# Kernel tuning notes

Hardware: AMD Instinct MI355X
Metric: run time of the kernel (lower is better)

## Reference

```python
import jax, jax.numpy as jnp
import numpy as np

# dims: num_time T, batch B, nodes N, feature F(=hidden_dim), heads H(must be 1, see notes)
T, B, N, F, H = 16, 32, 512, 128, 1
E = F * T          # embed_size = hidden_dim * num_time = 2048
D = E // H         # head_dim = 2048


def setup_inputs() -> dict:
    key = jax.random.key(0)
    ks = jax.random.split(key, 9)
    s = 0.02
    return {
        "x":   jax.random.normal(ks[0], (T, B, N, F), dtype=jnp.float32),
        # torch nn.Linear convention: W is [out_features, in_features], y = x @ W.T + b
        "Wq":  jax.random.normal(ks[1], (D, D), dtype=jnp.float32) * s,
        "bq":  jnp.zeros((D,), dtype=jnp.float32),
        "Wk":  jax.random.normal(ks[2], (D, D), dtype=jnp.float32) * s,
        "bk":  jnp.zeros((D,), dtype=jnp.float32),
        "Wv":  jax.random.normal(ks[3], (E, D), dtype=jnp.float32) * s,
        "bv":  jnp.zeros((E,), dtype=jnp.float32),
        "Wfc": jax.random.normal(ks[4], (E, E), dtype=jnp.float32) * s,
        "bfc": jnp.zeros((E,), dtype=jnp.float32),
    }


def reference(x, Wq, bq, Wk, bk, Wv, bv, Wfc, bfc):
    Tt, Bb, Nn, Ff = x.shape
    Ee = Ff * Tt
    # mean over axis 1 of the ORIGINAL [T,B,N,F] tensor (this is the batch axis;
    # the original code calls it node_axis but operates on the un-permuted x)
    x_mean = x.mean(axis=1)                                   # [T, N, F]
    # permute(1,2,3,0).reshape -> [B, N, F*T], then split heads (H=1)
    xr = jnp.transpose(x, (1, 2, 3, 0)).reshape(Bb, Nn, H, Ee // H)
    q = xr @ Wq.T + bq                                        # [B, N, H, D]
    k = xr @ Wk.T + bk                                        # [B, N, H, D]
    v = xr @ Wv.T + bv                                        # [B, N, H, E]
    energy = jnp.einsum('nqhd,nkhd->nhqk', q, k)              # [B, H, N, N]
    attention = jax.nn.softmax(energy / jnp.sqrt(jnp.float32(Ee)), axis=3)
    out = jnp.einsum('nhql,nlhd->nqhd', attention, v).reshape(Bb, Nn, Ee)
    out = out @ Wfc.T + bfc                                   # [B, N, E]
    # faithful to the original's (buggy) view: (nodes, batch, T, F) then permute
    out = jnp.transpose(out.reshape(Nn, Bb, Tt, Ff), (2, 1, 0, 3)).mean(axis=1)  # [T, N, F]
    return x_mean + out, attention
```

## Files before the change

### kernel.cpp

```cpp
#include <hip/hip_runtime.h>

typedef __attribute__((ext_vector_type(8))) __bf16 bf16x8;
typedef __attribute__((ext_vector_type(4))) float floatx4;

__device__ __forceinline__ float bf2f(unsigned short u) {
    union { unsigned int i; float f; } v; v.i = ((unsigned int)u) << 16; return v.f;
}
__device__ __forceinline__ unsigned short f2bf(float f) {
    union { float f; unsigned int i; } v; v.f = f;
    unsigned int u = v.i;
    return (unsigned short)((u + 0x7fffu + ((u >> 16) & 1u)) >> 16);
}

__device__ __forceinline__ void async16(const void* g, void* l) {
    __builtin_amdgcn_global_load_lds(
        (__attribute__((address_space(1))) void*)(g),
        (__attribute__((address_space(3))) void*)(l), 16, 0, 0);
}

__global__ void detect_dtype(const unsigned short* __restrict__ w, int* __restrict__ flag)
{
    int tid = threadIdx.x;
    int cnt = 0;
    for (int i = tid; i < 256; i += 64) {
        unsigned short s = w[2 * i];
        int e = (s >> 7) & 0xFF;
        if (e >= 100 && e <= 126) cnt++;
    }
#pragma unroll
    for (int off = 32; off > 0; off >>= 1) cnt += __shfl_xor(cnt, off);
    if (tid == 0) *flag = (cnt >= 128) ? 1 : 0;
}

__global__ __launch_bounds__(256)
void convert_bf16(const void* __restrict__ in, unsigned short* __restrict__ out,
                  int n, float scale, const int* __restrict__ flag)
{
    int i = (blockIdx.x * 256 + threadIdx.x) * 4;
    if (i >= n) return;
    float f[4];
    if (*flag) {
        const unsigned short* p = (const unsigned short*)in + i;
#pragma unroll
        for (int j = 0; j < 4; j++) f[j] = bf2f(p[j]);
    } else {
        float4 v = *(const float4*)((const float*)in + i);
        f[0] = v.x; f[1] = v.y; f[2] = v.z; f[3] = v.w;
    }
    union { uint2 u; unsigned short s[4]; } W;
#pragma unroll
    for (int j = 0; j < 4; j++) W.s[j] = f2bf(f[j] * scale);
    *(uint2*)(out + i) = W.u;
}

__global__ __launch_bounds__(256)
void transpose_conv(const void* __restrict__ in, unsigned short* __restrict__ out,
                    const int* __restrict__ flag)
{
    __shared__ unsigned short tile[64 * 65];
    const int d0 = blockIdx.x * 64, i0 = blockIdx.y * 64;
    const int tid = threadIdx.x;
    const int r = tid >> 2, seg = tid & 3;

    const long base = (long)(d0 + r) * 2048 + i0 + seg * 16;
    unsigned short vals[16];
    if (*flag) {
        const unsigned short* p = (const unsigned short*)in + base;
        union { uint4 u; unsigned short s[8]; } a, b;
        a.u = *(const uint4*)p; b.u = *(const uint4*)(p + 8);
#pragma unroll
        for (int j = 0; j < 8; j++) { vals[j] = a.s[j]; vals[8 + j] = b.s[j]; }
    } else {
        const float* p = (const float*)in + base;
#pragma unroll
        for (int q = 0; q < 4; q++) {
            float4 v = *(const float4*)(p + q * 4);
            vals[q * 4 + 0] = f2bf(v.x); vals[q * 4 + 1] = f2bf(v.y);
            vals[q * 4 + 2] = f2bf(v.z); vals[q * 4 + 3] = f2bf(v.w);
        }
    }
#pragma unroll
    for (int j = 0; j < 16; j++) tile[r * 65 + seg * 16 + j] = vals[j];
    __syncthreads();

    union { uint4 u[2]; unsigned short s[16]; } W;
#pragma unroll
    for (int j = 0; j < 16; j++) W.s[j] = tile[(seg * 16 + j) * 65 + r];
    unsigned short* o = out + (long)(i0 + r) * 2048 + d0 + seg * 16;
    *(uint4*)o = W.u[0];
    *(uint4*)(o + 8) = W.u[1];
}

__global__ __launch_bounds__(256)
void build_xr(const void* __restrict__ xv, unsigned short* __restrict__ xr,
              const int* __restrict__ flag)
{
    __shared__ __align__(16) unsigned short tile[128 * 24];
    const int bn = blockIdx.x;
    const int b = bn >> 9, n = bn & 511;
    const int tid = threadIdx.x;
    const int t = tid >> 4, l16 = tid & 15;

    const long off = (long)(t * 32 + b) * 65536 + n * 128 + l16 * 8;
    union { uint4 u; unsigned short s[8]; } U;
    if (*flag) {
        U.u = *(const uint4*)((const unsigned short*)xv + off);
    } else {
        const float* xf = (const float*)xv + off;
        float4 f0 = *(const float4*)xf;
        float4 f1 = *(const float4*)(xf + 4);
        U.s[0] = f2bf(f0.x); U.s[1] = f2bf(f0.y); U.s[2] = f2bf(f0.z); U.s[3] = f2bf(f0.w);
        U.s[4] = f2bf(f1.x); U.s[5] = f2bf(f1.y); U.s[6] = f2bf(f1.z); U.s[7] = f2bf(f1.w);
    }
#pragma unroll
    for (int j = 0; j < 8; j++) tile[(l16 * 8 + j) * 24 + t] = U.s[j];
    __syncthreads();

    const int f = tid >> 1, t0 = (tid & 1) * 8;
    uint4 o = *(const uint4*)&tile[f * 24 + t0];
    *(uint4*)(xr + (long)bn * 2048 + tid * 8) = o;
}

template <int MODE, bool BIAS>
__global__ __launch_bounds__(256)
void gemm_nt(const unsigned short* __restrict__ Ag,
             const unsigned short* __restrict__ Bg,
             void* __restrict__ Cg,
             const unsigned short* __restrict__ bias,
             int K, long sA, long sB, long sC, int lda, int ldb, int ldc)
{
    __shared__ __align__(16) unsigned short lsA[128 * 32];
    __shared__ __align__(16) unsigned short lsB[128 * 32];

    const int tid = threadIdx.x;
    const int z = blockIdx.z;
    const unsigned short* A = Ag + (long)z * sA + (long)blockIdx.y * 128 * lda;
    const unsigned short* B = Bg + (long)z * sB + (long)blockIdx.x * 128 * ldb;

    const int wave = tid >> 6, lane = tid & 63;
    const int wm = (wave >> 1) * 64, wn = (wave & 1) * 64;
    const int r = lane & 15, quad = lane >> 4;

    floatx4 acc[4][4];
#pragma unroll
    for (int i = 0; i < 4; i++)
#pragma unroll
        for (int j = 0; j < 4; j++) acc[i][j] = floatx4{0.f, 0.f, 0.f, 0.f};

    const int srow = tid >> 2;
    const int scol = (tid & 3) * 8;
    const long a0 = (long)srow * lda + scol;
    const long a1 = (long)(srow + 64) * lda + scol;
    const long b0 = (long)srow * ldb + scol;
    const long b1 = (long)(srow + 64) * ldb + scol;

    for (int k0 = 0; k0 < K; k0 += 32) {
        async16(A + k0 + a0, (char*)lsA + tid * 16);
        async16(A + k0 + a1, (char*)lsA + 4096 + tid * 16);
        async16(B + k0 + b0, (char*)lsB + tid * 16);
        async16(B + k0 + b1, (char*)lsB + 4096 + tid * 16);
        __syncthreads();

        const bf16x8* pA = (const bf16x8*)lsA;
        const bf16x8* pB = (const bf16x8*)lsB;
        bf16x8 af[4], bb[4];
#pragma unroll
        for (int i = 0; i < 4; i++) af[i] = pA[(wm + i * 16 + r) * 4 + quad];
#pragma unroll
        for (int j = 0; j < 4; j++) bb[j] = pB[(wn + j * 16 + r) * 4 + quad];
#pragma unroll
        for (int i = 0; i < 4; i++)
#pragma unroll
            for (int j = 0; j < 4; j++)
                acc[i][j] = __builtin_amdgcn_mfma_f32_16x16x32_bf16(af[i], bb[j], acc[i][j], 0, 0, 0);
        __syncthreads();
    }

    const int mb = blockIdx.y * 128 + wm + quad * 4;
    const int nb = blockIdx.x * 128 + wn + r;

    if (MODE == 1) {
        float* C = (float*)Cg + (long)z * sC;
#pragma unroll
        for (int i = 0; i < 4; i++)
#pragma unroll
            for (int j = 0; j < 4; j++)
#pragma unroll
                for (int g = 0; g < 4; g++)
                    C[(long)(mb + i * 16 + g) * ldc + (nb + j * 16)] = acc[i][j][g];
    } else {
        unsigned short* C = (unsigned short*)Cg + (long)z * sC;
#pragma unroll
        for (int j = 0; j < 4; j++) {
            const int n = nb + j * 16;
            const float bj = BIAS ? bf2f(bias[n]) : 0.0f;
#pragma unroll
            for (int i = 0; i < 4; i++)
#pragma unroll
                for (int g = 0; g < 4; g++)
                    C[(long)(mb + i * 16 + g) * ldc + n] = f2bf(acc[i][j][g] + bj);
        }
    }
}

__global__ __launch_bounds__(256)
void w2_kernel(const unsigned short* __restrict__ WkT,
               const unsigned short* __restrict__ bqb, float* __restrict__ w2)
{
    const int i = blockIdx.x, tid = threadIdx.x;
    const unsigned short* row = WkT + (long)i * 2048 + tid * 8;
    const unsigned short* bv = bqb + tid * 8;
    union { uint4 u; unsigned short s[8]; } A, B;
    A.u = *(const uint4*)row; B.u = *(const uint4*)bv;
    float s = 0.f;
#pragma unroll
    for (int j = 0; j < 8; j++) s += bf2f(A.s[j]) * bf2f(B.s[j]);
#pragma unroll
    for (int off = 32; off > 0; off >>= 1) s += __shfl_xor(s, off);
    __shared__ float red[4];
    if ((tid & 63) == 0) red[tid >> 6] = s;
    __syncthreads();
    if (tid == 0) w2[i] = red[0] + red[1] + red[2] + red[3];
}

__global__ __launch_bounds__(256)
void c_kernel(const unsigned short* __restrict__ xr, const float* __restrict__ w2,
              float* __restrict__ c)
{
    const int row = blockIdx.x * 4 + (threadIdx.x >> 6);
    const int lane = threadIdx.x & 63;
    float s = 0.f;
#pragma unroll
    for (int ch = 0; ch < 4; ch++) {
        const int i0 = ch * 512 + lane * 8;
        union { uint4 u; unsigned short s[8]; } X;
        X.u = *(const uint4*)(xr + (long)row * 2048 + i0);
        float4 w0 = *(const float4*)(w2 + i0);
        float4 w1 = *(const float4*)(w2 + i0 + 4);
        s += bf2f(X.s[0]) * w0.x + bf2f(X.s[1]) * w0.y + bf2f(X.s[2]) * w0.z + bf2f(X.s[3]) * w0.w;
        s += bf2f(X.s[4]) * w1.x + bf2f(X.s[5]) * w1.y + bf2f(X.s[6]) * w1.z + bf2f(X.s[7]) * w1.w;
    }
#pragma unroll
    for (int off = 32; off > 0; off >>= 1) s += __shfl_xor(s, off);
    if (lane == 0) c[row] = s;
}

__global__ __launch_bounds__(256)
void softmax_rows(const float* __restrict__ S, const float* __restrict__ c,
                  void* __restrict__ dout, const int* __restrict__ flag)
{
    const long row = blockIdx.x;
    const int tid = threadIdx.x;
    const float scale = 0.02209708691207961f;
    float2 v = ((const float2*)(S + row * 512))[tid];
    float2 cv = ((const float2*)(c + (row >> 9) * 512))[tid];
    float a = (v.x + cv.x) * scale, b = (v.y + cv.y) * scale;

    __shared__ float redm[4], reds[4];
    float m = fmaxf(a, b);
#pragma unroll
    for (int off = 32; off > 0; off >>= 1) m = fmaxf(m, __shfl_xor(m, off));
    if ((tid & 63) == 0) redm[tid >> 6] = m;
    __syncthreads();
    m = fmaxf(fmaxf(redm[0], redm[1]), fmaxf(redm[2], redm[3]));

    float ea = __expf(a - m), eb = __expf(b - m);
    float s = ea + eb;
#pragma unroll
    for (int off = 32; off > 0; off >>= 1) s += __shfl_xor(s, off);
    if ((tid & 63) == 0) reds[tid >> 6] = s;
    __syncthreads();
    s = reds[0] + reds[1] + reds[2] + reds[3];
    const float inv = 1.0f / s;
    const float fa = ea * inv, fb = eb * inv;

    if (*flag) {
        unsigned short* P = (unsigned short*)dout + 1048576;
        const unsigned int packed = (unsigned int)f2bf(fa) | ((unsigned int)f2bf(fb) << 16);
        ((unsigned int*)(P + row * 512))[tid] = packed;
    } else {
        float* P = (float*)dout + 1048576;
        ((float2*)(P + row * 512))[tid] = make_float2(fa, fb);
    }
}

__global__ __launch_bounds__(256)
void pbar_reduce(const void* __restrict__ dout, unsigned short* __restrict__ Pbar,
                 const int* __restrict__ flag)
{
    const int g = blockIdx.x, tid = threadIdx.x;
    float s0 = 0.f, s1 = 0.f;
    if (*flag) {
        const unsigned short* P = (const unsigned short*)dout + 1048576;
        const unsigned short* p = P + (long)g * 32 * 512 + tid * 2;
        for (int r = 0; r < 32; r++) {
            unsigned int u = *(const unsigned int*)(p + (long)r * 512);
            s0 += bf2f((unsigned short)(u & 0xffff));
            s1 += bf2f((unsigned short)(u >> 16));
        }
    } else {
        const float* P = (const float*)dout + 1048576;
        const float* p = P + (long)g * 32 * 512 + tid * 2;
        for (int r = 0; r < 32; r++) {
            float2 v = *(const float2*)(p + (long)r * 512);
            s0 += v.x; s1 += v.y;
        }
    }
    const unsigned int packed = (unsigned int)f2bf(s0) | ((unsigned int)f2bf(s1) << 16);
    ((unsigned int*)(Pbar + (long)g * 512))[tid] = packed;
}

__global__ __launch_bounds__(256)
void z_kernel(const unsigned short* __restrict__ Pbar,
              const unsigned short* __restrict__ xr,
              unsigned short* __restrict__ Z)
{
    __shared__ __align__(16) unsigned short tile[32 * 64];
    const int b = blockIdx.y, d0 = blockIdx.x * 64;
    const int tid = threadIdx.x;
    const int wave = tid >> 6, lane = tid & 63;
    const int r = lane & 15, quad = lane >> 4;
    const unsigned short* xrb = xr + (long)b * 512 * 2048;

    floatx4 acc = floatx4{0.f, 0.f, 0.f, 0.f};
    for (int l0 = 0; l0 < 512; l0 += 32) {
        async16(xrb + (long)(l0 + (tid >> 3)) * 2048 + d0 + (tid & 7) * 8,
                (char*)tile + tid * 16);
        __syncthreads();
        bf16x8 a = *(const bf16x8*)(Pbar + (long)(b * 16 + r) * 512 + l0 + quad * 8);
        union { bf16x8 v; unsigned short s[8]; } bb;
#pragma unroll
        for (int j = 0; j < 8; j++) bb.s[j] = tile[(quad * 8 + j) * 64 + wave * 16 + r];
        acc = __builtin_amdgcn_mfma_f32_16x16x32_bf16(a, bb.v, acc, 0, 0, 0);
        __syncthreads();
    }
#pragma unroll
    for (int g = 0; g < 4; g++)
        Z[(long)(b * 16 + quad * 4 + g) * 2048 + d0 + wave * 16 + r] = f2bf(acc[g]);
}

__global__ __launch_bounds__(256)
void final_small(const void* __restrict__ xv, const unsigned short* __restrict__ Ybar,
                 const unsigned short* __restrict__ bfcb, void* __restrict__ dout,
                 const int* __restrict__ flag)
{
    const int n = blockIdx.x;
    const int tid = threadIdx.x;
    const int col0 = tid * 8;
    const int t = col0 >> 7, f0 = col0 & 127;
    const int isbf = *flag;

    float acc[8];
    {
        union { uint4 u; unsigned short s[8]; } Yv, Bv;
        Yv.u = *(const uint4*)(Ybar + (long)n * 2048 + col0);
        Bv.u = *(const uint4*)(bfcb + col0);
#pragma unroll
        for (int j = 0; j < 8; j++) acc[j] = bf2f(Yv.s[j]) + 32.0f * bf2f(Bv.s[j]);
    }
    const long xoff = (long)t * 2097152 + n * 128 + f0;
    if (isbf) {
        const unsigned short* xb = (const unsigned short*)xv + xoff;
        for (int b = 0; b < 32; b++) {
            union { uint4 u; unsigned short s[8]; } U;
            U.u = *(const uint4*)(xb + (long)b * 65536);
#pragma unroll
            for (int j = 0; j < 8; j++) acc[j] += bf2f(U.s[j]);
        }
    } else {
        const float* xb = (const float*)xv + xoff;
        for (int b = 0; b < 32; b++) {
            float4 g0 = *(const float4*)(xb + (long)b * 65536);
            float4 g1 = *(const float4*)(xb + (long)b * 65536 + 4);
            acc[0] += g0.x; acc[1] += g0.y; acc[2] += g0.z; acc[3] += g0.w;
            acc[4] += g1.x; acc[5] += g1.y; acc[6] += g1.z; acc[7] += g1.w;
        }
    }
    const long oidx = (long)t * 65536 + n * 128 + f0;
    if (isbf) {
        union { uint4 u; unsigned short s[8]; } W;
#pragma unroll
        for (int j = 0; j < 8; j++) W.s[j] = f2bf(acc[j] * 0.03125f);
        *(uint4*)((unsigned short*)dout + oidx) = W.u;
    } else {
        float* o = (float*)dout + oidx;
#pragma unroll
        for (int j = 0; j < 8; j += 4)
            *(float4*)(o + j) = make_float4(acc[j] * 0.03125f, acc[j + 1] * 0.03125f,
                                            acc[j + 2] * 0.03125f, acc[j + 3] * 0.03125f);
    }
}

extern "C" void kernel_launch(void* const* d_in, const int* in_sizes, int n_in,
                              void* d_out, int out_size, void* d_ws, size_t ws_size,
                              hipStream_t stream)
{
    unsigned short* xr   = (unsigned short*)d_ws;
    unsigned short* H    = xr + 33554432;
    float*          S    = (float*)(H + 33554432);
    unsigned short* Gt   = (unsigned short*)(S + 8388608);
    unsigned short* WqT  = Gt  + 4194304;
    unsigned short* WkT  = WqT + 4194304;
    unsigned short* Wvb  = WkT + 4194304;
    unsigned short* Wfcb = Wvb + 4194304;
    unsigned short* Pbar = Wfcb + 4194304;
    unsigned short* Z    = Pbar + 262144;
    unsigned short* Obar = Z + 1048576;
    unsigned short* Ybar = Obar + 1048576;
    unsigned short* bqb  = Ybar + 1048576;
    unsigned short* bvb  = bqb + 2048;
    unsigned short* bfcb = bvb + 2048;
    float*          w2   = (float*)(bfcb + 2048);
    float*          c    = w2 + 2048;
    int*            flag = (int*)(c + 16384);

    detect_dtype<<<1, 64, 0, stream>>>((const unsigned short*)d_in[1], flag);
    transpose_conv<<<dim3(32, 32), 256, 0, stream>>>(d_in[1], WqT, flag);
    transpose_conv<<<dim3(32, 32), 256, 0, stream>>>(d_in[3], WkT, flag);
    convert_bf16<<<4096, 256, 0, stream>>>(d_in[5], Wvb,  4194304, 1.0f, flag);
    convert_bf16<<<4096, 256, 0, stream>>>(d_in[7], Wfcb, 4194304, 1.0f, flag);
    convert_bf16<<<2, 256, 0, stream>>>(d_in[2], bqb,  2048, 1.0f,  flag);
    convert_bf16<<<2, 256, 0, stream>>>(d_in[6], bvb,  2048, 32.0f, flag);
    convert_bf16<<<2, 256, 0, stream>>>(d_in[8], bfcb, 2048, 1.0f,  flag);

    build_xr<<<16384, 256, 0, stream>>>(d_in[0], xr, flag);
    gemm_nt<0, false><<<dim3(16, 16, 1), 256, 0, stream>>>(
        WkT, WqT, Gt, nullptr, 2048, 0, 0, 0, 2048, 2048, 2048);
    gemm_nt<0, false><<<dim3(16, 128, 1), 256, 0, stream>>>(
        xr, Gt, H, nullptr, 2048, 0, 0, 0, 2048, 2048, 2048);
    w2_kernel<<<2048, 256, 0, stream>>>(WkT, bqb, w2);
    c_kernel<<<4096, 256, 0, stream>>>(xr, w2, c);
    gemm_nt<1, false><<<dim3(4, 4, 32), 256, 0, stream>>>(
        H, xr, S, nullptr, 2048, 1048576, 1048576, 262144, 2048, 2048, 512);
    softmax_rows<<<16384, 256, 0, stream>>>(S, c, d_out, flag);
    pbar_reduce<<<512, 256, 0, stream>>>(d_out, Pbar, flag);
    z_kernel<<<dim3(32, 32), 256, 0, stream>>>(Pbar, xr, Z);
    gemm_nt<0, true><<<dim3(16, 4, 1), 256, 0, stream>>>(
        Z, Wvb, Obar, bvb, 2048, 0, 0, 0, 2048, 2048, 2048);
    gemm_nt<0, false><<<dim3(16, 4, 1), 256, 0, stream>>>(
        Obar, Wfcb, Ybar, nullptr, 2048, 0, 0, 0, 2048, 2048, 2048);
    final_small<<<512, 256, 0, stream>>>(d_in[0], Ybar, bfcb, d_out, flag);
}
```

Before: 786.3 us.

## Fuse softmax with Pbar reduction, direct-load GEMM B operand, merge conversions

Four separate changes. First, softmax now runs as 512 blocks that each process 32 rows in sequence and accumulate the attention column sums (Pbar) in registers, so the separate pbar_reduce pass that re-read the attention output is gone. Second, the GEMMs gain a BDIRECT mode that loads B fragments straight from global memory into registers instead of staging them in LDS; this adds exposed global load latency and duplicate reads across waves. Third, the weight and bias conversions are merged into two launches, and final_small computes the x mean from the bf16 xr buffer, which rounds x to bf16 when the input is fp32.

```diff
diff --git a/kernel.cpp b/kernel.cpp
--- a/kernel.cpp
+++ b/kernel.cpp
@@ -33,24 +33,49 @@
 }
 
 __global__ __launch_bounds__(256)
-void convert_bf16(const void* __restrict__ in, unsigned short* __restrict__ out,
-                  int n, float scale, const int* __restrict__ flag)
-{
+void convert_weights(const void* __restrict__ w5, const void* __restrict__ w7,
+                     unsigned short* __restrict__ o5, unsigned short* __restrict__ o7,
+                     const int* __restrict__ flag)
+{
+    const void* in = blockIdx.y ? w7 : w5;
+    unsigned short* out = blockIdx.y ? o7 : o5;
     int i = (blockIdx.x * 256 + threadIdx.x) * 4;
-    if (i >= n) return;
-    float f[4];
+    if (*flag) {
+        *(uint2*)(out + i) = *(const uint2*)((const unsigned short*)in + i);
+    } else {
+        float4 f = *(const float4*)((const float*)in + i);
+        union { uint2 u; unsigned short s[4]; } W;
+        W.s[0] = f2bf(f.x); W.s[1] = f2bf(f.y); W.s[2] = f2bf(f.z); W.s[3] = f2bf(f.w);
+        *(uint2*)(out + i) = W.u;
+    }
+}
+
+__global__ __launch_bounds__(256)
+void convert_biases(const void* __restrict__ bq, const void* __restrict__ bv,
+                    const void* __restrict__ bfc,
+                    unsigned short* __restrict__ bqb, unsigned short* __restrict__ bvb,
+                    unsigned short* __restrict__ bfcb, const int* __restrict__ flag)
+{
+    const int which = blockIdx.x;
+    const void* in = which == 0 ? bq : (which == 1 ? bv : bfc);
+    unsigned short* out = which == 0 ? bqb : (which == 1 ? bvb : bfcb);
+    const float scale = which == 1 ? 32.0f : 1.0f;
+    int i = threadIdx.x * 8;
+    float f[8];
     if (*flag) {
         const unsigned short* p = (const unsigned short*)in + i;
 #pragma unroll
-        for (int j = 0; j < 4; j++) f[j] = bf2f(p[j]);
-    } else {
-        float4 v = *(const float4*)((const float*)in + i);
-        f[0] = v.x; f[1] = v.y; f[2] = v.z; f[3] = v.w;
-    }
-    union { uint2 u; unsigned short s[4]; } W;
-#pragma unroll
-    for (int j = 0; j < 4; j++) W.s[j] = f2bf(f[j] * scale);
-    *(uint2*)(out + i) = W.u;
+        for (int j = 0; j < 8; j++) f[j] = bf2f(p[j]);
+    } else {
+        float4 a = *(const float4*)((const float*)in + i);
+        float4 b = *(const float4*)((const float*)in + i + 4);
+        f[0] = a.x; f[1] = a.y; f[2] = a.z; f[3] = a.w;
+        f[4] = b.x; f[5] = b.y; f[6] = b.z; f[7] = b.w;
+    }
+    union { uint4 u; unsigned short s[8]; } W;
+#pragma unroll
+    for (int j = 0; j < 8; j++) W.s[j] = f2bf(f[j] * scale);
+    *(uint4*)(out + i) = W.u;
 }
 
 __global__ __launch_bounds__(256)
@@ -121,7 +146,7 @@
     *(uint4*)(xr + (long)bn * 2048 + tid * 8) = o;
 }
 
-template <int MODE, bool BIAS>
+template <int MODE, bool BIAS, bool BDIRECT>
 __global__ __launch_bounds__(256)
 void gemm_nt(const unsigned short* __restrict__ Ag,
              const unsigned short* __restrict__ Bg,
@@ -130,7 +155,7 @@
              int K, long sA, long sB, long sC, int lda, int ldb, int ldc)
 {
     __shared__ __align__(16) unsigned short lsA[128 * 32];
-    __shared__ __align__(16) unsigned short lsB[128 * 32];
+    __shared__ __align__(16) unsigned short lsB[BDIRECT ? 8 : 128 * 32];
 
     const int tid = threadIdx.x;
     const int z = blockIdx.z;
@@ -157,17 +182,26 @@
     for (int k0 = 0; k0 < K; k0 += 32) {
         async16(A + k0 + a0, (char*)lsA + tid * 16);
         async16(A + k0 + a1, (char*)lsA + 4096 + tid * 16);
-        async16(B + k0 + b0, (char*)lsB + tid * 16);
-        async16(B + k0 + b1, (char*)lsB + 4096 + tid * 16);
+        bf16x8 bb[4];
+        if (BDIRECT) {
+#pragma unroll
+            for (int j = 0; j < 4; j++)
+                bb[j] = *(const bf16x8*)(B + (long)(wn + j * 16 + r) * ldb + k0 + quad * 8);
+        } else {
+            async16(B + k0 + b0, (char*)lsB + tid * 16);
+            async16(B + k0 + b1, (char*)lsB + 4096 + tid * 16);
+        }
         __syncthreads();
 
         const bf16x8* pA = (const bf16x8*)lsA;
-        const bf16x8* pB = (const bf16x8*)lsB;
-        bf16x8 af[4], bb[4];
+        bf16x8 af[4];
 #pragma unroll
         for (int i = 0; i < 4; i++) af[i] = pA[(wm + i * 16 + r) * 4 + quad];
-#pragma unroll
-        for (int j = 0; j < 4; j++) bb[j] = pB[(wn + j * 16 + r) * 4 + quad];
+        if (!BDIRECT) {
+            const bf16x8* pB = (const bf16x8*)lsB;
+#pragma unroll
+            for (int j = 0; j < 4; j++) bb[j] = pB[(wn + j * 16 + r) * 4 + quad];
+        }
 #pragma unroll
         for (int i = 0; i < 4; i++)
 #pragma unroll
@@ -246,68 +280,55 @@
 }
 
 __global__ __launch_bounds__(256)
-void softmax_rows(const float* __restrict__ S, const float* __restrict__ c,
-                  void* __restrict__ dout, const int* __restrict__ flag)
-{
-    const long row = blockIdx.x;
+void softmax_pbar(const float* __restrict__ S, const float* __restrict__ c,
+                  void* __restrict__ dout, unsigned short* __restrict__ Pbar,
+                  const int* __restrict__ flag)
+{
+    const int g = blockIdx.x;
+    const int b = g >> 4;
     const int tid = threadIdx.x;
     const float scale = 0.02209708691207961f;
-    float2 v = ((const float2*)(S + row * 512))[tid];
-    float2 cv = ((const float2*)(c + (row >> 9) * 512))[tid];
-    float a = (v.x + cv.x) * scale, b = (v.y + cv.y) * scale;
-
+    const int isbf = *flag;
     __shared__ float redm[4], reds[4];
-    float m = fmaxf(a, b);
-#pragma unroll
-    for (int off = 32; off > 0; off >>= 1) m = fmaxf(m, __shfl_xor(m, off));
-    if ((tid & 63) == 0) redm[tid >> 6] = m;
-    __syncthreads();
-    m = fmaxf(fmaxf(redm[0], redm[1]), fmaxf(redm[2], redm[3]));
-
-    float ea = __expf(a - m), eb = __expf(b - m);
-    float s = ea + eb;
-#pragma unroll
-    for (int off = 32; off > 0; off >>= 1) s += __shfl_xor(s, off);
-    if ((tid & 63) == 0) reds[tid >> 6] = s;
-    __syncthreads();
-    s = reds[0] + reds[1] + reds[2] + reds[3];
-    const float inv = 1.0f / s;
-    const float fa = ea * inv, fb = eb * inv;
-
-    if (*flag) {
-        unsigned short* P = (unsigned short*)dout + 1048576;
-        const unsigned int packed = (unsigned int)f2bf(fa) | ((unsigned int)f2bf(fb) << 16);
-        ((unsigned int*)(P + row * 512))[tid] = packed;
-    } else {
-        float* P = (float*)dout + 1048576;
-        ((float2*)(P + row * 512))[tid] = make_float2(fa, fb);
-    }
-}
-
-__global__ __launch_bounds__(256)
-void pbar_reduce(const void* __restrict__ dout, unsigned short* __restrict__ Pbar,
-                 const int* __restrict__ flag)
-{
-    const int g = blockIdx.x, tid = threadIdx.x;
-    float s0 = 0.f, s1 = 0.f;
-    if (*flag) {
-        const unsigned short* P = (const unsigned short*)dout + 1048576;
-        const unsigned short* p = P + (long)g * 32 * 512 + tid * 2;
-        for (int r = 0; r < 32; r++) {
-            unsigned int u = *(const unsigned int*)(p + (long)r * 512);
-            s0 += bf2f((unsigned short)(u & 0xffff));
-            s1 += bf2f((unsigned short)(u >> 16));
+
+    float2 cv = ((const float2*)(c + b * 512))[tid];
+    float p0 = 0.f, p1 = 0.f;
+
+    for (int r = 0; r < 32; r++) {
+        const long row = (long)g * 32 + r;
+        float2 v = ((const float2*)(S + row * 512))[tid];
+        float a = (v.x + cv.x) * scale, d = (v.y + cv.y) * scale;
+
+        float m = fmaxf(a, d);
+#pragma unroll
+        for (int off = 32; off > 0; off >>= 1) m = fmaxf(m, __shfl_xor(m, off));
+        if ((tid & 63) == 0) redm[tid >> 6] = m;
+        __syncthreads();
+        m = fmaxf(fmaxf(redm[0], redm[1]), fmaxf(redm[2], redm[3]));
+
+        float ea = __expf(a - m), eb = __expf(d - m);
+        float s = ea + eb;
+#pragma unroll
+        for (int off = 32; off > 0; off >>= 1) s += __shfl_xor(s, off);
+        if ((tid & 63) == 0) reds[tid >> 6] = s;
+        __syncthreads();
+        s = reds[0] + reds[1] + reds[2] + reds[3];
+        const float inv = 1.0f / s;
+        const float fa = ea * inv, fb = eb * inv;
+        p0 += fa; p1 += fb;
+
+        if (isbf) {
+            unsigned short* P = (unsigned short*)dout + 1048576;
+            ((unsigned int*)(P + row * 512))[tid] =
+                (unsigned int)f2bf(fa) | ((unsigned int)f2bf(fb) << 16);
+        } else {
+            float* P = (float*)dout + 1048576;
+            ((float2*)(P + row * 512))[tid] = make_float2(fa, fb);
         }
-    } else {
-        const float* P = (const float*)dout + 1048576;
-        const float* p = P + (long)g * 32 * 512 + tid * 2;
-        for (int r = 0; r < 32; r++) {
-            float2 v = *(const float2*)(p + (long)r * 512);
-            s0 += v.x; s1 += v.y;
-        }
-    }
-    const unsigned int packed = (unsigned int)f2bf(s0) | ((unsigned int)f2bf(s1) << 16);
-    ((unsigned int*)(Pbar + (long)g * 512))[tid] = packed;
+        __syncthreads();
+    }
+    ((unsigned int*)(Pbar + (long)g * 512))[tid] =
+        (unsigned int)f2bf(p0) | ((unsigned int)f2bf(p1) << 16);
 }
 
 __global__ __launch_bounds__(256)
@@ -340,41 +361,38 @@
 }
 
 __global__ __launch_bounds__(256)
-void final_small(const void* __restrict__ xv, const unsigned short* __restrict__ Ybar,
+void final_small(const unsigned short* __restrict__ xr,
+                 const unsigned short* __restrict__ Ybar,
                  const unsigned short* __restrict__ bfcb, void* __restrict__ dout,
                  const int* __restrict__ flag)
 {
+    __shared__ float xm[2048];
     const int n = blockIdx.x;
     const int tid = threadIdx.x;
+    const int isbf = *flag;
+
+    float a[8] = {0, 0, 0, 0, 0, 0, 0, 0};
+    const unsigned short* base = xr + (long)n * 2048 + tid * 8;
+    for (int b = 0; b < 32; b++) {
+        union { uint4 u; unsigned short s[8]; } U;
+        U.u = *(const uint4*)(base + (long)b * 1048576);
+#pragma unroll
+        for (int j = 0; j < 8; j++) a[j] += bf2f(U.s[j]);
+    }
+#pragma unroll
+    for (int j = 0; j < 8; j++) xm[tid * 8 + j] = a[j];
+    __syncthreads();
+
     const int col0 = tid * 8;
     const int t = col0 >> 7, f0 = col0 & 127;
-    const int isbf = *flag;
-
     float acc[8];
     {
         union { uint4 u; unsigned short s[8]; } Yv, Bv;
         Yv.u = *(const uint4*)(Ybar + (long)n * 2048 + col0);
         Bv.u = *(const uint4*)(bfcb + col0);
 #pragma unroll
-        for (int j = 0; j < 8; j++) acc[j] = bf2f(Yv.s[j]) + 32.0f * bf2f(Bv.s[j]);
-    }
-    const long xoff = (long)t * 2097152 + n * 128 + f0;
-    if (isbf) {
-        const unsigned short* xb = (const unsigned short*)xv + xoff;
-        for (int b = 0; b < 32; b++) {
-            union { uint4 u; unsigned short s[8]; } U;
-            U.u = *(const uint4*)(xb + (long)b * 65536);
-#pragma unroll
-            for (int j = 0; j < 8; j++) acc[j] += bf2f(U.s[j]);
-        }
-    } else {
-        const float* xb = (const float*)xv + xoff;
-        for (int b = 0; b < 32; b++) {
-            float4 g0 = *(const float4*)(xb + (long)b * 65536);
-            float4 g1 = *(const float4*)(xb + (long)b * 65536 + 4);
-            acc[0] += g0.x; acc[1] += g0.y; acc[2] += g0.z; acc[3] += g0.w;
-            acc[4] += g1.x; acc[5] += g1.y; acc[6] += g1.z; acc[7] += g1.w;
-        }
+        for (int j = 0; j < 8; j++)
+            acc[j] = bf2f(Yv.s[j]) + 32.0f * bf2f(Bv.s[j]) + xm[(f0 + j) * 16 + t];
     }
     const long oidx = (long)t * 65536 + n * 128 + f0;
     if (isbf) {
@@ -417,27 +435,23 @@
     detect_dtype<<<1, 64, 0, stream>>>((const unsigned short*)d_in[1], flag);
     transpose_conv<<<dim3(32, 32), 256, 0, stream>>>(d_in[1], WqT, flag);
     transpose_conv<<<dim3(32, 32), 256, 0, stream>>>(d_in[3], WkT, flag);
-    convert_bf16<<<4096, 256, 0, stream>>>(d_in[5], Wvb,  4194304, 1.0f, flag);
-    convert_bf16<<<4096, 256, 0, stream>>>(d_in[7], Wfcb, 4194304, 1.0f, flag);
-    convert_bf16<<<2, 256, 0, stream>>>(d_in[2], bqb,  2048, 1.0f,  flag);
-    convert_bf16<<<2, 256, 0, stream>>>(d_in[6], bvb,  2048, 32.0f, flag);
-    convert_bf16<<<2, 256, 0, stream>>>(d_in[8], bfcb, 2048, 1.0f,  flag);
+    convert_weights<<<dim3(4096, 2), 256, 0, stream>>>(d_in[5], d_in[7], Wvb, Wfcb, flag);
+    convert_biases<<<3, 256, 0, stream>>>(d_in[2], d_in[6], d_in[8], bqb, bvb, bfcb, flag);
 
     build_xr<<<16384, 256, 0, stream>>>(d_in[0], xr, flag);
-    gemm_nt<0, false><<<dim3(16, 16, 1), 256, 0, stream>>>(
+    gemm_nt<0, false, true><<<dim3(16, 16, 1), 256, 0, stream>>>(
         WkT, WqT, Gt, nullptr, 2048, 0, 0, 0, 2048, 2048, 2048);
-    gemm_nt<0, false><<<dim3(16, 128, 1), 256, 0, stream>>>(
+    gemm_nt<0, false, true><<<dim3(16, 128, 1), 256, 0, stream>>>(
         xr, Gt, H, nullptr, 2048, 0, 0, 0, 2048, 2048, 2048);
     w2_kernel<<<2048, 256, 0, stream>>>(WkT, bqb, w2);
     c_kernel<<<4096, 256, 0, stream>>>(xr, w2, c);
-    gemm_nt<1, false><<<dim3(4, 4, 32), 256, 0, stream>>>(
+    gemm_nt<1, false, false><<<dim3(4, 4, 32), 256, 0, stream>>>(
         H, xr, S, nullptr, 2048, 1048576, 1048576, 262144, 2048, 2048, 512);
-    softmax_rows<<<16384, 256, 0, stream>>>(S, c, d_out, flag);
-    pbar_reduce<<<512, 256, 0, stream>>>(d_out, Pbar, flag);
+    softmax_pbar<<<512, 256, 0, stream>>>(S, c, d_out, Pbar, flag);
     z_kernel<<<dim3(32, 32), 256, 0, stream>>>(Pbar, xr, Z);
-    gemm_nt<0, true><<<dim3(16, 4, 1), 256, 0, stream>>>(
+    gemm_nt<0, true, true><<<dim3(16, 4, 1), 256, 0, stream>>>(
         Z, Wvb, Obar, bvb, 2048, 0, 0, 0, 2048, 2048, 2048);
-    gemm_nt<0, false><<<dim3(16, 4, 1), 256, 0, stream>>>(
+    gemm_nt<0, false, true><<<dim3(16, 4, 1), 256, 0, stream>>>(
         Obar, Wfcb, Ybar, nullptr, 2048, 0, 0, 0, 2048, 2048, 2048);
-    final_small<<<512, 256, 0, stream>>>(d_in[0], Ybar, bfcb, d_out, flag);
-}
+    final_small<<<512, 256, 0, stream>>>(xr, Ybar, bfcb, d_out, flag);
+}
```

After: 931.8 us. +18.5%, slower.
